# Kernel tuning notes

Measured on AMD Instinct MI355X. Metric: run time of the kernel, lower is better.

Reference implementation:

```python
import jax, jax.numpy as jnp
import numpy as np

BSZ, L, D, K = 4, 4096, 512, 4


def setup_inputs() -> dict:
    key = jax.random.key(0)
    ks = jax.random.split(key, 8)
    n = jnp.arange(D, dtype=jnp.float32)
    f = jnp.sqrt(2.0 * n + 1.0)
    f = f / f.max()
    omega = jnp.exp(-f * np.float32(np.log(10000.0)))  # hippo_freqs(D)
    # freqs are strictly decreasing in n -> argsort descending == arange
    band_idx = jnp.argsort(-omega).reshape(K, D // K).astype(jnp.int32)
    B_vec = jnp.sqrt(2.0 * n + 1.0)
    B_vec = B_vec / B_vec.max()  # hippo_b_vector(D)
    return {
        "x": jax.random.normal(ks[0], (BSZ, L, D), dtype=jnp.float32),
        "z_prev": jax.random.normal(ks[1], (BSZ, L, D), dtype=jnp.float32),
        "W_psi": jax.random.normal(ks[2], (2 * D, D), dtype=jnp.float32) * 0.02,
        "b_psi": jnp.zeros((2 * D,), jnp.float32),
        "W_phi": jax.random.normal(ks[3], (2 * D, D), dtype=jnp.float32) * 0.02,
        "b_phi": jnp.zeros((2 * D,), jnp.float32),
        "W_gate": jax.random.normal(ks[4], (1, D), dtype=jnp.float32) * 0.02,
        "b_gate": jnp.zeros((1,), jnp.float32),
        "omega": omega,
        "log_gamma": jax.random.normal(ks[5], (D,), dtype=jnp.float32) - 3.0,
        "dt": jnp.array(0.1, jnp.float32),
        "surprise_gain": jnp.zeros((1,), jnp.float32),
        "tau": jnp.ones((1,), jnp.float32),
        "beta": jnp.zeros((1,), jnp.float32),
        "B_vec": B_vec,
        "band_idx": band_idx,
    }


def _exact_projection(z):
    # geodesic projection to zero-mean unit-std along last axis
    m = z.mean(-1, keepdims=True)
    v = ((z - m) ** 2).mean(-1, keepdims=True)
    return (z - m) / (jnp.sqrt(v) + 1e-6)


def reference(x, z_prev, W_psi, b_psi, W_phi, b_phi, W_gate, b_gate,
              omega, log_gamma, dt, surprise_gain, tau, beta, B_vec, band_idx):
    B_, L_, D_ = x.shape
    K_ = band_idx.shape[0]

    psi_raw = x @ W_psi.T + b_psi          # [B,L,2D]
    psi = jax.lax.complex(psi_raw[..., :D_], psi_raw[..., D_:])
    phi_raw = x @ W_phi.T + b_phi
    phi = jax.lax.complex(phi_raw[..., :D_], phi_raw[..., D_:])

    gate = jax.nn.sigmoid(x @ W_gate.T + b_gate)          # [B,L,1]
    surprise = jnp.abs(x - z_prev).mean(-1, keepdims=True)
    gate = gate * (1.0 + jnp.tanh(surprise_gain) * surprise)

    U = (gate * B_vec).astype(jnp.complex64) * psi        # [B,L,D] complex

    dta = jnp.abs(dt)
    lam = jax.lax.complex(-jnp.exp(log_gamma), omega)     # [D]
    t = jnp.arange(L_, dtype=jnp.float32)
    kernel = jnp.exp(lam[None, :] * (t[:, None] * dta))   # [L,D] complex, A^t

    n_fft = 2 * L_
    K_freq = jnp.fft.fft(kernel.T, n=n_fft, axis=1)                 # [D,2L]
    U_freq = jnp.fft.fft(jnp.transpose(U, (0, 2, 1)), n=n_fft, axis=2)  # [B,D,2L]
    H = jnp.fft.ifft(U_freq * K_freq[None], axis=2)[:, :, :L_]
    H = jnp.transpose(H, (0, 2, 1))                        # [B,L,D] complex

    H_proj = jax.lax.complex(_exact_projection(H.real), _exact_projection(H.imag))

    Hb = H_proj[:, :, band_idx]   # [B,L,K,band]
    Pb = phi[:, :, band_idx]
    alpha = (jnp.conj(Hb) * Pb).sum(-1, keepdims=True) / (D_ // K_)  # [B,L,K,1]
    c_k = jax.nn.softmax(jnp.abs(alpha) / jnp.clip(tau, 1e-4, None), axis=2)
    alpha_ig = alpha * c_k * K_
    density = (Hb.real ** 2 + Hb.imag ** 2).mean(-1, keepdims=True)
    alpha_fin = alpha_ig + (beta * density).astype(alpha_ig.dtype)
    out_bands = (Hb * alpha_fin).real                      # [B,L,K,band]

    out = jnp.zeros((B_, L_, D_), x.dtype).at[:, :, band_idx].set(out_bands)
    return out
```

## Files before the change

### kernel.cpp

```cpp
#include <hip/hip_runtime.h>
#include <hip/hip_bf16.h>
#include <math.h>

#define BSZ   4
#define LSEQ  4096
#define DDIM  512
#define KBAND 4
#define MROWS (BSZ*LSEQ)
#define BLD   (MROWS*DDIM)
#define CHUNK 64
#define NCH   (LSEQ/CHUNK)
#define NCOLS 2048

typedef __attribute__((ext_vector_type(8))) short  short8;
typedef __attribute__((ext_vector_type(8))) unsigned short u16x8;
typedef __attribute__((ext_vector_type(4))) float  f32x4;

__device__ __forceinline__ unsigned short f2bf(float f) {
    unsigned int u = __float_as_uint(f);
    u = (u + 0x7FFFu + ((u >> 16) & 1u)) >> 16;
    return (unsigned short)u;
}
__device__ __forceinline__ float bf2f(unsigned short h) {
    return __uint_as_float(((unsigned int)h) << 16);
}

__device__ __forceinline__ void gld_lds16(const void* g, void* l) {
    __builtin_amdgcn_global_load_lds(
        (const __attribute__((address_space(1))) void*)g,
        (__attribute__((address_space(3))) void*)l, 16, 0, 0);
}

__global__ void k_prep(const float* __restrict__ omega,
                       const float* __restrict__ log_gamma,
                       const float* __restrict__ dt,
                       const int*   __restrict__ band_idx,
                       float* __restrict__ apR, float* __restrict__ apI,
                       int* __restrict__ bandOf, int* __restrict__ posOf)
{
    int gid = blockIdx.x * blockDim.x + threadIdx.x;
    float dta = fabsf(dt[0]);
    if (gid < (CHUNK+1)*DDIM) {
        int k = gid / DDIM, d = gid % DDIM;
        float g = -expf(log_gamma[d]);
        float w = omega[d];
        float e = expf(g * dta * (float)k);
        float s, c;
        sincosf(w * dta * (float)k, &s, &c);
        apR[gid] = e * c;
        apI[gid] = e * s;
    }
    if (gid < DDIM) {
        int d = band_idx[gid];
        bandOf[d] = gid >> 7;
        posOf[d]  = gid & 127;
    }
}

__global__ void k_gate(const float* __restrict__ x,
                       const float* __restrict__ z_prev,
                       const float* __restrict__ Wg,
                       const float* __restrict__ bg,
                       const float* __restrict__ sg,
                       float* __restrict__ gate)
{
    int row  = blockIdx.x * 4 + (threadIdx.x >> 6);
    int lane = threadIdx.x & 63;
    const float4* xr = (const float4*)(x      + (size_t)row * DDIM);
    const float4* zr = (const float4*)(z_prev + (size_t)row * DDIM);
    const float4* wg = (const float4*)Wg;
    float dot = 0.f, sur = 0.f;
#pragma unroll
    for (int i = 0; i < 2; i++) {
        float4 a = xr[lane + i*64];
        float4 z = zr[lane + i*64];
        float4 w = wg[lane + i*64];
        dot += a.x*w.x + a.y*w.y + a.z*w.z + a.w*w.w;
        sur += fabsf(a.x-z.x) + fabsf(a.y-z.y) + fabsf(a.z-z.z) + fabsf(a.w-z.w);
    }
#pragma unroll
    for (int m = 32; m; m >>= 1) { dot += __shfl_xor(dot, m); sur += __shfl_xor(sur, m); }
    if (lane == 0) {
        float g = 1.f / (1.f + expf(-(dot + bg[0])));
        g *= (1.f + tanhf(sg[0]) * (sur * (1.f/512.f)));
        gate[row] = g;
    }
}

__global__ void k_cvtA(const float* __restrict__ x,
                       unsigned short* __restrict__ Ahi,
                       unsigned short* __restrict__ Alo)
{
    int gid = blockIdx.x * 256 + threadIdx.x;
    int m = gid >> 6, grp = gid & 63;
    int chunk = grp >> 3, g = grp & 7;
    int se = chunk*64 + ((g ^ (m & 7)) << 3);
    const float* xp = x + ((size_t)m << 9) + se;
    u16x8 h, l;
#pragma unroll
    for (int j = 0; j < 8; ++j) {
        float f = xp[j];
        unsigned short hb = f2bf(f);
        h[j] = hb;
        l[j] = f2bf(f - bf2f(hb));
    }
    size_t dst = ((size_t)m << 9) + grp*8;
    *(u16x8*)(Ahi + dst) = h;
    *(u16x8*)(Alo + dst) = l;
}

__global__ void k_cvtB(const float* __restrict__ Wpsi,
                       const float* __restrict__ Wphi,
                       unsigned short* __restrict__ Bhi,
                       unsigned short* __restrict__ Blo)
{
    int gid = blockIdx.x * 256 + threadIdx.x;
    int n = gid >> 6, grp = gid & 63;
    int chunk = grp >> 3, g = grp & 7;
    int se = chunk*64 + ((g ^ (n & 7)) << 3);
    const float* wp = (n < 1024) ? (Wpsi + ((size_t)n << 9) + se)
                                 : (Wphi + ((size_t)(n - 1024) << 9) + se);
    u16x8 h, l;
#pragma unroll
    for (int j = 0; j < 8; ++j) {
        float f = wp[j];
        unsigned short hb = f2bf(f);
        h[j] = hb;
        l[j] = f2bf(f - bf2f(hb));
    }
    size_t dst = ((size_t)n << 9) + grp*8;
    *(u16x8*)(Bhi + dst) = h;
    *(u16x8*)(Blo + dst) = l;
}

__global__ __launch_bounds__(256)
void k_gemm_bf16(const unsigned short* __restrict__ Ahi,
                 const unsigned short* __restrict__ Alo,
                 const unsigned short* __restrict__ Bhi,
                 const unsigned short* __restrict__ Blo,
                 const float* __restrict__ bpsi, const float* __restrict__ bphi,
                 float* __restrict__ psiR, float* __restrict__ psiI,
                 float* __restrict__ phiR, float* __restrict__ phiI)
{
    __shared__ __align__(16) char As[16384];
    __shared__ __align__(16) char Bs[16384];

    int bid = blockIdx.x;
    int wg  = (bid & 7) * 256 + (bid >> 3);
    int m0 = (wg >> 4) * 128;
    int n0 = (wg & 15) * 128;

    int tid  = threadIdx.x;
    int lane = tid & 63;
    int wv   = tid >> 6;
    int wm = wv >> 1, wn = wv & 1;
    int lr = lane & 15, lk = lane >> 4;

    f32x4 acc[4][4];
#pragma unroll
    for (int mi = 0; mi < 4; ++mi)
#pragma unroll
        for (int ni = 0; ni < 4; ++ni) acc[mi][ni] = (f32x4)0.f;

    for (int s = 0; s < 24; ++s) {
        const unsigned short* Asrc = (s >= 8 && s < 16) ? Alo : Ahi;
        const unsigned short* Bsrc = (s < 16) ? Bhi : Blo;
        int kb2 = (s & 7) << 7;

        __syncthreads();
#pragma unroll
        for (int i = 0; i < 4; ++i) {
            int flat = tid + i * 256;
            int r = flat >> 3, g = flat & 7;
            size_t goff = ((size_t)r << 10) + kb2 + g * 16;
            char* ldst = (char*)(void*)( (char*)0 );  (void)ldst;
            gld_lds16((const char*)Asrc + ((size_t)m0 << 10) + goff,
                      As + (wv * 64 + i * 256) * 16);
            gld_lds16((const char*)Bsrc + ((size_t)n0 << 10) + goff,
                      Bs + (wv * 64 + i * 256) * 16);
        }
        __syncthreads();

#pragma unroll
        for (int kk = 0; kk < 2; ++kk) {
            int tb = (kk * 64 + lk * 16) ^ ((lr & 7) << 4);
            short8 af[4], bfr[4];
#pragma unroll
            for (int mi = 0; mi < 4; ++mi) {
                int r = wm * 64 + mi * 16 + lr;
                af[mi] = *(const short8*)(As + r * 128 + tb);
            }
#pragma unroll
            for (int ni = 0; ni < 4; ++ni) {
                int r = wn * 64 + ni * 16 + lr;
                bfr[ni] = *(const short8*)(Bs + r * 128 + tb);
            }
#pragma unroll
            for (int mi = 0; mi < 4; ++mi)
#pragma unroll
                for (int ni = 0; ni < 4; ++ni)
                    acc[mi][ni] = __builtin_amdgcn_mfma_f32_16x16x32_bf16(
                        af[mi], bfr[ni], acc[mi][ni], 0, 0, 0);
        }
    }

#pragma unroll
    for (int ni = 0; ni < 4; ++ni) {
        int ncol = n0 + wn * 64 + ni * 16 + lr;
        float bias = (ncol < 1024) ? bpsi[ncol] : bphi[ncol - 1024];
        int p = ncol >> 9;
        float* plane = (p == 0) ? psiR : (p == 1) ? psiI : (p == 2) ? phiR : phiI;
        int col = ncol & 511;
#pragma unroll
        for (int mi = 0; mi < 4; ++mi) {
            int mrow = m0 + wm * 64 + mi * 16 + lk * 4;
#pragma unroll
            for (int j = 0; j < 4; ++j)
                plane[(size_t)(mrow + j) * 512 + col] = acc[mi][ni][j] + bias;
        }
    }
}

__launch_bounds__(512)
__global__ void k_scan(float* __restrict__ HR, float* __restrict__ HI,
                       const float* __restrict__ gate,
                       const float* __restrict__ Bvec,
                       const float* __restrict__ apR, const float* __restrict__ apI,
                       float* __restrict__ carR, float* __restrict__ carI)
{
    int b = blockIdx.x >> 6;
    int c = blockIdx.x & 63;
    int d = threadIdx.x;
    float ar = apR[DDIM + d], ai = apI[DDIM + d];
    float bv = Bvec[d];
    float hr = 0.f, hi = 0.f;
    int t0 = c * CHUNK;
    size_t base = ((size_t)b * LSEQ + t0) * DDIM + d;
    const float* grow = gate + (size_t)b * LSEQ + t0;
#pragma unroll 4
    for (int t = 0; t < CHUNK; t++) {
        float pr = HR[base], pi = HI[base];
        float g  = grow[t] * bv;
        float ur = g * pr, ui = g * pi;
        float nr = ar*hr - ai*hi + ur;
        float ni = ar*hi + ai*hr + ui;
        hr = nr; hi = ni;
        HR[base] = hr; HI[base] = hi;
        base += DDIM;
    }
    size_t ci = ((size_t)(b * NCH + c)) * DDIM + d;
    carR[ci] = hr; carI[ci] = hi;
}

__global__ void k_carry(float* __restrict__ carR, float* __restrict__ carI,
                        const float* __restrict__ apR, const float* __restrict__ apI)
{
    int gid = blockIdx.x * blockDim.x + threadIdx.x;
    int b = gid >> 9, d = gid & 511;
    float dr = apR[CHUNK*DDIM + d], di = apI[CHUNK*DDIM + d];
    size_t i0 = ((size_t)(b * NCH)) * DDIM + d;
    float cr = carR[i0], ci = carI[i0];
    for (int c = 1; c < NCH; c++) {
        size_t idx = i0 + (size_t)c * DDIM;
        float xr = carR[idx], xi = carI[idx];
        float nr = dr*cr - di*ci + xr;
        float ni = dr*ci + di*cr + xi;
        cr = nr; ci = ni;
        carR[idx] = cr; carI[idx] = ci;
    }
}

__device__ __forceinline__ float2 blockSum2(float a, float b, float* red)
{
#pragma unroll
    for (int m = 32; m; m >>= 1) { a += __shfl_xor(a, m); b += __shfl_xor(b, m); }
    int tid = threadIdx.x, w = tid >> 6;
    if ((tid & 63) == 0) { red[w*2] = a; red[w*2+1] = b; }
    __syncthreads();
    a = 0.f; b = 0.f;
#pragma unroll
    for (int i = 0; i < 8; i++) { a += red[i*2]; b += red[i*2+1]; }
    __syncthreads();
    return make_float2(a, b);
}

__launch_bounds__(512)
__global__ void k_out(const float* __restrict__ HR, const float* __restrict__ HI,
                      const float* __restrict__ phR, const float* __restrict__ phI,
                      const float* __restrict__ carR, const float* __restrict__ carI,
                      const float* __restrict__ apR, const float* __restrict__ apI,
                      const int* __restrict__ bandOf, const int* __restrict__ posOf,
                      const float* __restrict__ tau, const float* __restrict__ beta,
                      float* __restrict__ out)
{
    __shared__ float sA[512], sB[512], sC[512];
    __shared__ float pA[8], pB[8], pC[8];
    __shared__ float red[16];

    int bt = blockIdx.x;
    int b = bt >> 12, t = bt & 4095;
    int d = threadIdx.x;
    size_t idx = (size_t)bt * DDIM + d;

    float hr = HR[idx], hi = HI[idx];
    int c = t >> 6, off = t & 63;
    if (c > 0) {
        size_t ci = ((size_t)(b * NCH + (c - 1))) * DDIM + d;
        float cr = carR[ci], cm = carI[ci];
        float pr = apR[(off + 1) * DDIM + d], pi = apI[(off + 1) * DDIM + d];
        hr += pr*cr - pi*cm;
        hi += pr*cm + pi*cr;
    }
    float2 s = blockSum2(hr, hi, red);
    float mr = s.x * (1.f/512.f), mi = s.y * (1.f/512.f);
    float dr = hr - mr, di = hi - mi;
    float2 v = blockSum2(dr*dr, di*di, red);
    float Hpr = dr / (sqrtf(v.x * (1.f/512.f)) + 1e-6f);
    float Hpi = di / (sqrtf(v.y * (1.f/512.f)) + 1e-6f);

    float pr_ = phR[idx], pi_ = phI[idx];
    float ar_ = Hpr*pr_ + Hpi*pi_;
    float ai_ = Hpr*pi_ - Hpi*pr_;
    float dn_ = Hpr*Hpr + Hpi*Hpi;

    int kb = bandOf[d], jb = posOf[d];
    sA[kb*128 + jb] = ar_;
    sB[kb*128 + jb] = ai_;
    sC[kb*128 + jb] = dn_;
    __syncthreads();

    float v0 = sA[d], v1 = sB[d], v2 = sC[d];
#pragma unroll
    for (int m = 32; m; m >>= 1) {
        v0 += __shfl_xor(v0, m); v1 += __shfl_xor(v1, m); v2 += __shfl_xor(v2, m);
    }
    int w = d >> 6;
    if ((d & 63) == 0) { pA[w] = v0; pB[w] = v1; pC[w] = v2; }
    __syncthreads();

    float tv = tau[0]; tv = (tv < 1e-4f) ? 1e-4f : tv;
    float bt_s = beta[0];
    float aRk[4], aIk[4], dnk[4], mag[4];
    float mx = -1e30f;
#pragma unroll
    for (int k = 0; k < 4; k++) {
        aRk[k] = (pA[2*k] + pA[2*k+1]) * (1.f/128.f);
        aIk[k] = (pB[2*k] + pB[2*k+1]) * (1.f/128.f);
        dnk[k] = (pC[2*k] + pC[2*k+1]) * (1.f/128.f);
        mag[k] = sqrtf(aRk[k]*aRk[k] + aIk[k]*aIk[k]) / tv;
        mx = fmaxf(mx, mag[k]);
    }
    float se = 0.f, ek[4];
#pragma unroll
    for (int k = 0; k < 4; k++) { ek[k] = expf(mag[k] - mx); se += ek[k]; }
    float inv = 1.f / se;

    int kd = kb;
    float ck  = ek[kd] * inv;
    float afR = aRk[kd] * ck * 4.f + bt_s * dnk[kd];
    float afI = aIk[kd] * ck * 4.f;
    out[idx] = Hpr * afR - Hpi * afI;
}

extern "C" void kernel_launch(void* const* d_in, const int* in_sizes, int n_in,
                              void* d_out, int out_size, void* d_ws, size_t ws_size,
                              hipStream_t stream)
{
    const float* x        = (const float*)d_in[0];
    const float* z_prev   = (const float*)d_in[1];
    const float* W_psi    = (const float*)d_in[2];
    const float* b_psi    = (const float*)d_in[3];
    const float* W_phi    = (const float*)d_in[4];
    const float* b_phi    = (const float*)d_in[5];
    const float* W_gate   = (const float*)d_in[6];
    const float* b_gate   = (const float*)d_in[7];
    const float* omega    = (const float*)d_in[8];
    const float* log_gam  = (const float*)d_in[9];
    const float* dt       = (const float*)d_in[10];
    const float* sg       = (const float*)d_in[11];
    const float* tau      = (const float*)d_in[12];
    const float* beta     = (const float*)d_in[13];
    const float* B_vec    = (const float*)d_in[14];
    const int*   band_idx = (const int*)d_in[15];
    float* out = (float*)d_out;
    float* ws  = (float*)d_ws;

    float* psiR = ws;
    float* psiI = psiR + BLD;
    float* phiR = psiI + BLD;
    float* phiI = phiR + BLD;
    float* gate = phiI + BLD;
    float* apR  = gate + MROWS;
    float* apI  = apR + (CHUNK+1)*DDIM;
    float* carR = apI + (CHUNK+1)*DDIM;
    float* carI = carR + BSZ*NCH*DDIM;
    int* bandOf = (int*)(carI + BSZ*NCH*DDIM);
    int* posOf  = bandOf + DDIM;
    unsigned short* Bhi = (unsigned short*)(posOf + DDIM);
    unsigned short* Blo = Bhi + (size_t)NCOLS*512;

    unsigned short* Ahi = (unsigned short*)d_out;
    unsigned short* Alo = Ahi + (size_t)MROWS*512;

    k_prep<<<((CHUNK+1)*DDIM + 255)/256, 256, 0, stream>>>(
        omega, log_gam, dt, band_idx, apR, apI, bandOf, posOf);

    k_gate<<<MROWS/4, 256, 0, stream>>>(x, z_prev, W_gate, b_gate, sg, gate);

    k_cvtA<<<(MROWS*64)/256, 256, 0, stream>>>(x, Ahi, Alo);
    k_cvtB<<<(NCOLS*64)/256, 256, 0, stream>>>(W_psi, W_phi, Bhi, Blo);

    k_gemm_bf16<<<(MROWS/128) * (NCOLS/128), 256, 0, stream>>>(
        Ahi, Alo, Bhi, Blo, b_psi, b_phi, psiR, psiI, phiR, phiI);

    k_scan<<<BSZ * NCH, 512, 0, stream>>>(psiR, psiI, gate, B_vec, apR, apI, carR, carI);

    k_carry<<<(BSZ*DDIM)/256, 256, 0, stream>>>(carR, carI, apR, apI);

    k_out<<<MROWS, 512, 0, stream>>>(psiR, psiI, phiR, phiI, carR, carI,
                                     apR, apI, bandOf, posOf, tau, beta, out);
}
```

Before: 413.8 us.

## Shrink scan chunks and add hierarchical carry propagation; fuse gate with A conversion

Cuts the scan chunk length from 64 to 16, giving four times as many scan blocks to fill the GPU. The single serial carry pass is replaced by a three-level scheme: a local carry within groups of 16 chunks, a scan across group carries, and a parallel fix-up that uses a new table of decay powers at 16-step strides. Separately, the gate and surprise reduction is fused with the bf16 hi/lo split of x, so x is read once instead of twice. The cost is two extra small kernel launches and more carry traffic.

Result: no change. 412.5 us (-0.3%).

```diff
diff --git a/kernel.cpp b/kernel.cpp
--- a/kernel.cpp
+++ b/kernel.cpp
@@ -8,12 +8,15 @@
 #define KBAND 4
 #define MROWS (BSZ*LSEQ)
 #define BLD   (MROWS*DDIM)
-#define CHUNK 64
+#define CHUNK 16
 #define NCH   (LSEQ/CHUNK)
+#define NGRP  16
+#define TBL   ((CHUNK+1)*DDIM)
 #define NCOLS 2048
 
 typedef __attribute__((ext_vector_type(8))) short  short8;
 typedef __attribute__((ext_vector_type(8))) unsigned short u16x8;
+typedef __attribute__((ext_vector_type(4))) unsigned short u16x4;
 typedef __attribute__((ext_vector_type(4))) float  f32x4;
 
 __device__ __forceinline__ unsigned short f2bf(float f) {
@@ -36,11 +39,12 @@
                        const float* __restrict__ dt,
                        const int*   __restrict__ band_idx,
                        float* __restrict__ apR, float* __restrict__ apI,
+                       float* __restrict__ apgR, float* __restrict__ apgI,
                        int* __restrict__ bandOf, int* __restrict__ posOf)
 {
     int gid = blockIdx.x * blockDim.x + threadIdx.x;
     float dta = fabsf(dt[0]);
-    if (gid < (CHUNK+1)*DDIM) {
+    if (gid < TBL) {
         int k = gid / DDIM, d = gid % DDIM;
         float g = -expf(log_gamma[d]);
         float w = omega[d];
@@ -49,6 +53,17 @@
         sincosf(w * dta * (float)k, &s, &c);
         apR[gid] = e * c;
         apI[gid] = e * s;
+    } else if (gid < 2*TBL) {
+        int gg = gid - TBL;
+        int k = gg / DDIM, d = gg % DDIM;
+        float g = -expf(log_gamma[d]);
+        float w = omega[d];
+        float ph = dta * (float)(16 * k);
+        float e = expf(g * ph);
+        float s, c;
+        sincosf(w * ph, &s, &c);
+        apgR[gg] = e * c;
+        apgI[gg] = e * s;
     }
     if (gid < DDIM) {
         int d = band_idx[gid];
@@ -57,56 +72,52 @@
     }
 }
 
-__global__ void k_gate(const float* __restrict__ x,
-                       const float* __restrict__ z_prev,
-                       const float* __restrict__ Wg,
-                       const float* __restrict__ bg,
-                       const float* __restrict__ sg,
-                       float* __restrict__ gate)
-{
-    int row  = blockIdx.x * 4 + (threadIdx.x >> 6);
+__global__ void k_cvtgate(const float* __restrict__ x,
+                          const float* __restrict__ z_prev,
+                          const float* __restrict__ Wg,
+                          const float* __restrict__ bg,
+                          const float* __restrict__ sg,
+                          float* __restrict__ gate,
+                          unsigned short* __restrict__ Ahi,
+                          unsigned short* __restrict__ Alo)
+{
+    int m    = blockIdx.x * 4 + (threadIdx.x >> 6);
     int lane = threadIdx.x & 63;
-    const float4* xr = (const float4*)(x      + (size_t)row * DDIM);
-    const float4* zr = (const float4*)(z_prev + (size_t)row * DDIM);
+    const float4* xr = (const float4*)(x      + ((size_t)m << 9));
+    const float4* zr = (const float4*)(z_prev + ((size_t)m << 9));
     const float4* wg = (const float4*)Wg;
     float dot = 0.f, sur = 0.f;
+    int msw = m & 7;
 #pragma unroll
     for (int i = 0; i < 2; i++) {
-        float4 a = xr[lane + i*64];
-        float4 z = zr[lane + i*64];
-        float4 w = wg[lane + i*64];
+        int e = lane + i*64;
+        float4 a = xr[e];
+        float4 z = zr[e];
+        float4 w = wg[e];
         dot += a.x*w.x + a.y*w.y + a.z*w.z + a.w*w.w;
         sur += fabsf(a.x-z.x) + fabsf(a.y-z.y) + fabsf(a.z-z.z) + fabsf(a.w-z.w);
-    }
-#pragma unroll
-    for (int m = 32; m; m >>= 1) { dot += __shfl_xor(dot, m); sur += __shfl_xor(sur, m); }
+        float fa[4] = {a.x, a.y, a.z, a.w};
+        u16x4 h, l;
+#pragma unroll
+        for (int j = 0; j < 4; ++j) {
+            unsigned short hb = f2bf(fa[j]);
+            h[j] = hb;
+            l[j] = f2bf(fa[j] - bf2f(hb));
+        }
+        int grp = e >> 1, half = e & 1;
+        int chunk = grp >> 3, gs = grp & 7;
+        int gd = gs ^ msw;
+        size_t dst = ((size_t)m << 9) + chunk*64 + gd*8 + half*4;
+        *(u16x4*)(Ahi + dst) = h;
+        *(u16x4*)(Alo + dst) = l;
+    }
+#pragma unroll
+    for (int mm = 32; mm; mm >>= 1) { dot += __shfl_xor(dot, mm); sur += __shfl_xor(sur, mm); }
     if (lane == 0) {
         float g = 1.f / (1.f + expf(-(dot + bg[0])));
         g *= (1.f + tanhf(sg[0]) * (sur * (1.f/512.f)));
-        gate[row] = g;
-    }
-}
-
-__global__ void k_cvtA(const float* __restrict__ x,
-                       unsigned short* __restrict__ Ahi,
-                       unsigned short* __restrict__ Alo)
-{
-    int gid = blockIdx.x * 256 + threadIdx.x;
-    int m = gid >> 6, grp = gid & 63;
-    int chunk = grp >> 3, g = grp & 7;
-    int se = chunk*64 + ((g ^ (m & 7)) << 3);
-    const float* xp = x + ((size_t)m << 9) + se;
-    u16x8 h, l;
-#pragma unroll
-    for (int j = 0; j < 8; ++j) {
-        float f = xp[j];
-        unsigned short hb = f2bf(f);
-        h[j] = hb;
-        l[j] = f2bf(f - bf2f(hb));
-    }
-    size_t dst = ((size_t)m << 9) + grp*8;
-    *(u16x8*)(Ahi + dst) = h;
-    *(u16x8*)(Alo + dst) = l;
+        gate[m] = g;
+    }
 }
 
 __global__ void k_cvtB(const float* __restrict__ Wpsi,
@@ -173,7 +184,6 @@
             int flat = tid + i * 256;
             int r = flat >> 3, g = flat & 7;
             size_t goff = ((size_t)r << 10) + kb2 + g * 16;
-            char* ldst = (char*)(void*)( (char*)0 );  (void)ldst;
             gld_lds16((const char*)Asrc + ((size_t)m0 << 10) + goff,
                       As + (wv * 64 + i * 256) * 16);
             gld_lds16((const char*)Bsrc + ((size_t)n0 << 10) + goff,
@@ -228,8 +238,8 @@
                        const float* __restrict__ apR, const float* __restrict__ apI,
                        float* __restrict__ carR, float* __restrict__ carI)
 {
-    int b = blockIdx.x >> 6;
-    int c = blockIdx.x & 63;
+    int b = blockIdx.x >> 8;
+    int c = blockIdx.x & 255;
     int d = threadIdx.x;
     float ar = apR[DDIM + d], ai = apI[DDIM + d];
     float bv = Bvec[d];
@@ -237,7 +247,7 @@
     int t0 = c * CHUNK;
     size_t base = ((size_t)b * LSEQ + t0) * DDIM + d;
     const float* grow = gate + (size_t)b * LSEQ + t0;
-#pragma unroll 4
+#pragma unroll
     for (int t = 0; t < CHUNK; t++) {
         float pr = HR[base], pi = HI[base];
         float g  = grow[t] * bv;
@@ -252,22 +262,64 @@
     carR[ci] = hr; carI[ci] = hi;
 }
 
-__global__ void k_carry(float* __restrict__ carR, float* __restrict__ carI,
-                        const float* __restrict__ apR, const float* __restrict__ apI)
-{
-    int gid = blockIdx.x * blockDim.x + threadIdx.x;
-    int b = gid >> 9, d = gid & 511;
-    float dr = apR[CHUNK*DDIM + d], di = apI[CHUNK*DDIM + d];
-    size_t i0 = ((size_t)(b * NCH)) * DDIM + d;
+__global__ void k_carryA(float* __restrict__ carR, float* __restrict__ carI,
+                         const float* __restrict__ apR, const float* __restrict__ apI)
+{
+    int gid = blockIdx.x * 256 + threadIdx.x;
+    int d = gid & 511, cg = (gid >> 9) & 15, b = gid >> 13;
+    float qr = apR[CHUNK*DDIM + d], qi = apI[CHUNK*DDIM + d];
+    size_t i0 = ((size_t)(b * NCH + cg * 16)) * DDIM + d;
     float cr = carR[i0], ci = carI[i0];
-    for (int c = 1; c < NCH; c++) {
-        size_t idx = i0 + (size_t)c * DDIM;
-        float xr = carR[idx], xi = carI[idx];
-        float nr = dr*cr - di*ci + xr;
-        float ni = dr*ci + di*cr + xi;
+#pragma unroll
+    for (int j = 1; j < 16; j++) {
+        float xr = carR[i0 + (size_t)j * DDIM];
+        float xi = carI[i0 + (size_t)j * DDIM];
+        float nr = qr*cr - qi*ci + xr;
+        float ni = qr*ci + qi*cr + xi;
         cr = nr; ci = ni;
-        carR[idx] = cr; carI[idx] = ci;
-    }
+        carR[i0 + (size_t)j * DDIM] = cr;
+        carI[i0 + (size_t)j * DDIM] = ci;
+    }
+}
+
+__global__ void k_carryB(const float* __restrict__ carR, const float* __restrict__ carI,
+                         const float* __restrict__ apgR, const float* __restrict__ apgI,
+                         float* __restrict__ gcarR, float* __restrict__ gcarI)
+{
+    int gid = blockIdx.x * 256 + threadIdx.x;
+    int d = gid & 511, b = gid >> 9;
+    float Qr = apgR[16*DDIM + d], Qi = apgI[16*DDIM + d];
+    size_t base = ((size_t)(b * NCH + 15)) * DDIM + d;
+    float gr = carR[base], gi = carI[base];
+    gcarR[((size_t)(b*NGRP))*DDIM + d] = gr;
+    gcarI[((size_t)(b*NGRP))*DDIM + d] = gi;
+#pragma unroll
+    for (int cg = 1; cg < NGRP; cg++) {
+        size_t idx = ((size_t)(b * NCH + cg*16 + 15)) * DDIM + d;
+        float tr = carR[idx], ti = carI[idx];
+        float nr = Qr*gr - Qi*gi + tr;
+        float ni = Qr*gi + Qi*gr + ti;
+        gr = nr; gi = ni;
+        gcarR[((size_t)(b*NGRP + cg))*DDIM + d] = gr;
+        gcarI[((size_t)(b*NGRP + cg))*DDIM + d] = gi;
+    }
+}
+
+__global__ void k_carryC(float* __restrict__ carR, float* __restrict__ carI,
+                         const float* __restrict__ apgR, const float* __restrict__ apgI,
+                         const float* __restrict__ gcarR, const float* __restrict__ gcarI)
+{
+    int gid = blockIdx.x * 256 + threadIdx.x;
+    int d = gid & 511, c = (gid >> 9) & 255, b = gid >> 17;
+    int cg = c >> 4;
+    if (cg == 0) return;
+    int jj = c & 15;
+    float fr = apgR[(jj+1)*DDIM + d], fi = apgI[(jj+1)*DDIM + d];
+    size_t gidx = ((size_t)(b*NGRP + cg - 1))*DDIM + d;
+    float gr = gcarR[gidx], gi = gcarI[gidx];
+    size_t idx = ((size_t)(b * NCH + c)) * DDIM + d;
+    carR[idx] += fr*gr - fi*gi;
+    carI[idx] += fr*gi + fi*gr;
 }
 
 __device__ __forceinline__ float2 blockSum2(float a, float b, float* red)
@@ -303,7 +355,7 @@
     size_t idx = (size_t)bt * DDIM + d;
 
     float hr = HR[idx], hi = HI[idx];
-    int c = t >> 6, off = t & 63;
+    int c = t >> 4, off = t & 15;
     if (c > 0) {
         size_t ci = ((size_t)(b * NCH + (c - 1))) * DDIM + d;
         float cr = carR[ci], cm = carI[ci];
@@ -391,10 +443,14 @@
     float* phiI = phiR + BLD;
     float* gate = phiI + BLD;
     float* apR  = gate + MROWS;
-    float* apI  = apR + (CHUNK+1)*DDIM;
-    float* carR = apI + (CHUNK+1)*DDIM;
-    float* carI = carR + BSZ*NCH*DDIM;
-    int* bandOf = (int*)(carI + BSZ*NCH*DDIM);
+    float* apI  = apR + TBL;
+    float* apgR = apI + TBL;
+    float* apgI = apgR + TBL;
+    float* carR = apgI + TBL;
+    float* carI = carR + (size_t)BSZ*NCH*DDIM;
+    float* gcarR = carI + (size_t)BSZ*NCH*DDIM;
+    float* gcarI = gcarR + (size_t)BSZ*NGRP*DDIM;
+    int* bandOf = (int*)(gcarI + (size_t)BSZ*NGRP*DDIM);
     int* posOf  = bandOf + DDIM;
     unsigned short* Bhi = (unsigned short*)(posOf + DDIM);
     unsigned short* Blo = Bhi + (size_t)NCOLS*512;
@@ -402,12 +458,12 @@
     unsigned short* Ahi = (unsigned short*)d_out;
     unsigned short* Alo = Ahi + (size_t)MROWS*512;
 
-    k_prep<<<((CHUNK+1)*DDIM + 255)/256, 256, 0, stream>>>(
-        omega, log_gam, dt, band_idx, apR, apI, bandOf, posOf);
-
-    k_gate<<<MROWS/4, 256, 0, stream>>>(x, z_prev, W_gate, b_gate, sg, gate);
-
-    k_cvtA<<<(MROWS*64)/256, 256, 0, stream>>>(x, Ahi, Alo);
+    k_prep<<<(2*TBL + 255)/256, 256, 0, stream>>>(
+        omega, log_gam, dt, band_idx, apR, apI, apgR, apgI, bandOf, posOf);
+
+    k_cvtgate<<<MROWS/4, 256, 0, stream>>>(x, z_prev, W_gate, b_gate, sg,
+                                           gate, Ahi, Alo);
+
     k_cvtB<<<(NCOLS*64)/256, 256, 0, stream>>>(W_psi, W_phi, Bhi, Blo);
 
     k_gemm_bf16<<<(MROWS/128) * (NCOLS/128), 256, 0, stream>>>(
@@ -415,7 +471,9 @@
 
     k_scan<<<BSZ * NCH, 512, 0, stream>>>(psiR, psiI, gate, B_vec, apR, apI, carR, carI);
 
-    k_carry<<<(BSZ*DDIM)/256, 256, 0, stream>>>(carR, carI, apR, apI);
+    k_carryA<<<(BSZ*NGRP*DDIM)/256, 256, 0, stream>>>(carR, carI, apR, apI);
+    k_carryB<<<(BSZ*DDIM)/256, 256, 0, stream>>>(carR, carI, apgR, apgI, gcarR, gcarI);
+    k_carryC<<<(BSZ*NCH*DDIM)/256, 256, 0, stream>>>(carR, carI, apgR, apgI, gcarR, gcarI);
 
     k_out<<<MROWS, 512, 0, stream>>>(psiR, psiI, phiR, phiI, carR, carI,
                                      apR, apI, bandOf, posOf, tau, beta, out);
```
